# Performance work log

Hardware: AMD Instinct MI355X
Metric: run time of the kernel (lower is better)

## Reference

```python
import jax, jax.numpy as jnp
import numpy as np

N_NODES = 50000
N_EDGES = 600000
IN_FEATS = 128
OUT_FEATS = 128


def setup_inputs() -> dict:
    key = jax.random.key(0)
    k1, k2, k3, k4, k5 = jax.random.split(key, 5)
    edge_row = jax.random.randint(k1, (N_EDGES,), 0, N_NODES, dtype=jnp.int32)
    edge_col = jax.random.randint(k2, (N_EDGES,), 0, N_NODES, dtype=jnp.int32)
    edge_vals = jax.random.uniform(k3, (N_EDGES,), dtype=jnp.float32)
    node_embs = jax.random.normal(k4, (N_NODES, IN_FEATS), dtype=jnp.float32)
    gcn_weight = jax.random.normal(k5, (IN_FEATS, OUT_FEATS), dtype=jnp.float32) / np.sqrt(IN_FEATS)
    return {"edge_row": edge_row, "edge_col": edge_col, "edge_vals": edge_vals,
            "node_embs": node_embs, "gcn_weight": gcn_weight}


def reference(edge_row, edge_col, edge_vals, node_embs, gcn_weight):
    # SpMM: Ahat @ node_embs, with Ahat in COO form (row, col, val)
    gathered = node_embs[edge_col] * edge_vals[:, None]          # [E, in_feats]
    agg = jax.ops.segment_sum(gathered, edge_row, num_segments=N_NODES)  # [N, in_feats]
    # dense GEMM + activation
    out = jax.nn.relu(agg @ gcn_weight)                          # [N, out_feats]
    return out
```

## Files before the change

kernel.cpp:

```cpp
#include <hip/hip_runtime.h>
#include <hip/hip_fp16.h>

#define NN 50000
#define NE 600000
#define F  128
#define CAP 128
#define NFILL_BLK 586
#define NGEMM_BLK 782

#define WS_NEEDED 64200064u

__global__ void k_zero4(int4* __restrict__ p, int n4) {
    int i = blockIdx.x * blockDim.x + threadIdx.x;
    if (i < n4) p[i] = make_int4(0, 0, 0, 0);
}

#define FMA4(ACC, AS, WV) \
    ACC.x += (AS) * WV.x; ACC.y += (AS) * WV.y; ACC.z += (AS) * WV.z; ACC.w += (AS) * WV.w;

__global__ __launch_bounds__(256) void k_gemm_fill(const float* __restrict__ X,
                                                   const float* __restrict__ W,
                                                   __half* __restrict__ XW,
                                                   const int4* __restrict__ erow4,
                                                   const int4* __restrict__ ecol4,
                                                   const float4* __restrict__ eval4,
                                                   int* __restrict__ cnt,
                                                   int2* __restrict__ pairs) {
    if (blockIdx.x < NFILL_BLK) {
        int t = blockIdx.x * 256 + threadIdx.x;
        if (t * 4 < NE) {
            int4   r4 = erow4[t];
            int4   c4 = ecol4[t];
            float4 v4 = eval4[t];
            int p0 = atomicAdd(&cnt[r4.x], 1);
            int p1 = atomicAdd(&cnt[r4.y], 1);
            int p2 = atomicAdd(&cnt[r4.z], 1);
            int p3 = atomicAdd(&cnt[r4.w], 1);
            if (p0 < CAP) pairs[(size_t)r4.x * CAP + p0] = make_int2(c4.x, __float_as_int(v4.x));
            if (p1 < CAP) pairs[(size_t)r4.y * CAP + p1] = make_int2(c4.y, __float_as_int(v4.y));
            if (p2 < CAP) pairs[(size_t)r4.z * CAP + p2] = make_int2(c4.z, __float_as_int(v4.z));
            if (p3 < CAP) pairs[(size_t)r4.w * CAP + p3] = make_int2(c4.w, __float_as_int(v4.w));
        }
        return;
    }
    __shared__ float Wl[64][128];
    __shared__ float Al[64][128];
    const int tid = threadIdx.x;
    const int rg  = tid >> 5;
    const int oq  = (tid & 31) << 2;
    const int row0 = (blockIdx.x - NFILL_BLK) * 64;

    #pragma unroll
    for (int i = 0; i < 8; ++i) {
        int idx4 = i * 256 + tid;
        int r  = idx4 >> 5;
        int cc = (idx4 & 31) << 2;
        int grow = row0 + r;
        float4 v = make_float4(0.f, 0.f, 0.f, 0.f);
        if (grow < NN)
            v = *reinterpret_cast<const float4*>(X + (size_t)grow * F + cc);
        *reinterpret_cast<float4*>(&Al[r][cc]) = v;
    }

    float4 acc[8];
    #pragma unroll
    for (int j = 0; j < 8; ++j) acc[j] = make_float4(0.f, 0.f, 0.f, 0.f);

    for (int kk = 0; kk < 2; ++kk) {
        if (kk) __syncthreads();
        #pragma unroll
        for (int i = 0; i < 8; ++i) {
            int idx4 = i * 256 + tid;
            *reinterpret_cast<float4*>(reinterpret_cast<float*>(Wl) + idx4 * 4) =
                *reinterpret_cast<const float4*>(W + kk * 64 * F + idx4 * 4);
        }
        __syncthreads();
        #pragma unroll 2
        for (int k4 = 0; k4 < 64; k4 += 4) {
            float4 w0 = *reinterpret_cast<const float4*>(&Wl[k4 + 0][oq]);
            float4 w1 = *reinterpret_cast<const float4*>(&Wl[k4 + 1][oq]);
            float4 w2 = *reinterpret_cast<const float4*>(&Wl[k4 + 2][oq]);
            float4 w3 = *reinterpret_cast<const float4*>(&Wl[k4 + 3][oq]);
            #pragma unroll
            for (int r = 0; r < 8; ++r) {
                float4 a = *reinterpret_cast<const float4*>(&Al[rg * 8 + r][kk * 64 + k4]);
                FMA4(acc[r], a.x, w0)
                FMA4(acc[r], a.y, w1)
                FMA4(acc[r], a.z, w2)
                FMA4(acc[r], a.w, w3)
            }
        }
    }
    #pragma unroll
    for (int r = 0; r < 8; ++r) {
        int grow = row0 + rg * 8 + r;
        if (grow < NN) {
            float4 a = acc[r];
            __half2 lo = __float22half2_rn(make_float2(a.x, a.y));
            __half2 hi = __float22half2_rn(make_float2(a.z, a.w));
            uint2 pk;
            pk.x = *reinterpret_cast<unsigned*>(&lo);
            pk.y = *reinterpret_cast<unsigned*>(&hi);
            *reinterpret_cast<uint2*>(XW + (size_t)grow * F + oq) = pk;
        }
    }
}

#define PGATH(I, ACC) { \
    int2 e = bp[(I) + half]; \
    float v = __int_as_float(e.y); \
    uint2 h4 = *reinterpret_cast<const uint2*>(XW + (size_t)e.x * F + (li << 2)); \
    float2 flo = __half22float2(*reinterpret_cast<__half2*>(&h4.x)); \
    float2 fhi = __half22float2(*reinterpret_cast<__half2*>(&h4.y)); \
    ACC.x += flo.x * v; ACC.y += flo.y * v; ACC.z += fhi.x * v; ACC.w += fhi.y * v; }

__global__ __launch_bounds__(256) void k_agg_relu(const int* __restrict__ cnt,
                                                  const int2* __restrict__ pairs,
                                                  const __half* __restrict__ XW,
                                                  float* __restrict__ out) {
    const int wid  = threadIdx.x >> 6;
    const int lane = threadIdx.x & 63;
    const int node = blockIdx.x * 4 + wid;
    if (node >= NN) return;
    int n = cnt[node];
    n = (n > CAP) ? CAP : n;
    const int2* bp = pairs + (size_t)node * CAP;
    const int half = lane >> 5;
    const int li   = lane & 31;

    float4 a0 = make_float4(0.f, 0.f, 0.f, 0.f), a1 = a0, a2 = a0, a3 = a0;
    int i = 0;
    for (; i + 8 <= n; i += 8) {
        PGATH(i + 0, a0) PGATH(i + 2, a1) PGATH(i + 4, a2) PGATH(i + 6, a3)
    }
    if (i + 4 <= n) { PGATH(i + 0, a0) PGATH(i + 2, a1) i += 4; }
    if (i + 2 <= n) { PGATH(i + 0, a2) i += 2; }
    if (i < n) {
        int2 e = bp[i];
        float v = (half == 0) ? __int_as_float(e.y) : 0.f;
        uint2 h4 = *reinterpret_cast<const uint2*>(XW + (size_t)e.x * F + (li << 2));
        float2 flo = __half22float2(*reinterpret_cast<__half2*>(&h4.x));
        float2 fhi = __half22float2(*reinterpret_cast<__half2*>(&h4.y));
        a3.x += flo.x * v; a3.y += flo.y * v; a3.z += fhi.x * v; a3.w += fhi.y * v;
    }
    float4 s;
    s.x = (a0.x + a1.x) + (a2.x + a3.x);
    s.y = (a0.y + a1.y) + (a2.y + a3.y);
    s.z = (a0.z + a1.z) + (a2.z + a3.z);
    s.w = (a0.w + a1.w) + (a2.w + a3.w);
    s.x += __shfl_xor(s.x, 32);
    s.y += __shfl_xor(s.y, 32);
    s.z += __shfl_xor(s.z, 32);
    s.w += __shfl_xor(s.w, 32);
    if (half == 0) {
        s.x = fmaxf(s.x, 0.f);
        s.y = fmaxf(s.y, 0.f);
        s.z = fmaxf(s.z, 0.f);
        s.w = fmaxf(s.w, 0.f);
        *reinterpret_cast<float4*>(out + (size_t)node * F + (li << 2)) = s;
    }
}

__global__ void k_zero_f4(float4* __restrict__ p, int n4) {
    int i = blockIdx.x * blockDim.x + threadIdx.x;
    if (i < n4) p[i] = make_float4(0.f, 0.f, 0.f, 0.f);
}

__global__ void k_scatter(const int* __restrict__ erow, const int* __restrict__ ecol,
                          const float* __restrict__ eval, const float* __restrict__ X,
                          float* __restrict__ agg) {
    unsigned tid = blockIdx.x * blockDim.x + threadIdx.x;
    unsigned e = tid >> 5;
    if (e >= NE) return;
    unsigned f = (tid & 31u) << 2;
    int   r = erow[e];
    int   c = ecol[e];
    float v = eval[e];
    float4 x = *reinterpret_cast<const float4*>(X + (size_t)c * F + f);
    float* dst = agg + (size_t)r * F + f;
    atomicAdd(dst + 0, x.x * v);
    atomicAdd(dst + 1, x.y * v);
    atomicAdd(dst + 2, x.z * v);
    atomicAdd(dst + 3, x.w * v);
}

__global__ __launch_bounds__(256) void k_gemm_relu(float* __restrict__ io,
                                                   const float* __restrict__ W) {
    __shared__ float Wl[64][128];
    __shared__ float Al[64][128];
    const int tid = threadIdx.x;
    const int rg  = tid >> 5;
    const int oq  = (tid & 31) << 2;
    const int row0 = blockIdx.x * 64;

    #pragma unroll
    for (int i = 0; i < 8; ++i) {
        int idx4 = i * 256 + tid;
        int r  = idx4 >> 5;
        int cc = (idx4 & 31) << 2;
        int grow = row0 + r;
        float4 v = make_float4(0.f, 0.f, 0.f, 0.f);
        if (grow < NN)
            v = *reinterpret_cast<const float4*>(io + (size_t)grow * F + cc);
        *reinterpret_cast<float4*>(&Al[r][cc]) = v;
    }
    float4 acc[8];
    #pragma unroll
    for (int j = 0; j < 8; ++j) acc[j] = make_float4(0.f, 0.f, 0.f, 0.f);
    for (int kk = 0; kk < 2; ++kk) {
        if (kk) __syncthreads();
        #pragma unroll
        for (int i = 0; i < 8; ++i) {
            int idx4 = i * 256 + tid;
            *reinterpret_cast<float4*>(reinterpret_cast<float*>(Wl) + idx4 * 4) =
                *reinterpret_cast<const float4*>(W + kk * 64 * F + idx4 * 4);
        }
        __syncthreads();
        #pragma unroll 2
        for (int k4 = 0; k4 < 64; k4 += 4) {
            float4 w0 = *reinterpret_cast<const float4*>(&Wl[k4 + 0][oq]);
            float4 w1 = *reinterpret_cast<const float4*>(&Wl[k4 + 1][oq]);
            float4 w2 = *reinterpret_cast<const float4*>(&Wl[k4 + 2][oq]);
            float4 w3 = *reinterpret_cast<const float4*>(&Wl[k4 + 3][oq]);
            #pragma unroll
            for (int r = 0; r < 8; ++r) {
                float4 a = *reinterpret_cast<const float4*>(&Al[rg * 8 + r][kk * 64 + k4]);
                FMA4(acc[r], a.x, w0)
                FMA4(acc[r], a.y, w1)
                FMA4(acc[r], a.z, w2)
                FMA4(acc[r], a.w, w3)
            }
        }
    }
    #pragma unroll
    for (int r = 0; r < 8; ++r) {
        int grow = row0 + rg * 8 + r;
        if (grow < NN) {
            float4 a = acc[r];
            a.x = fmaxf(a.x, 0.f);
            a.y = fmaxf(a.y, 0.f);
            a.z = fmaxf(a.z, 0.f);
            a.w = fmaxf(a.w, 0.f);
            *reinterpret_cast<float4*>(io + (size_t)grow * F + oq) = a;
        }
    }
}

extern "C" void kernel_launch(void* const* d_in, const int* in_sizes, int n_in,
                              void* d_out, int out_size, void* d_ws, size_t ws_size,
                              hipStream_t stream) {
    const int*   erow  = (const int*)d_in[0];
    const int*   ecol  = (const int*)d_in[1];
    const float* evals = (const float*)d_in[2];
    const float* X     = (const float*)d_in[3];
    const float* W     = (const float*)d_in[4];
    float* out = (float*)d_out;

    if (ws_size >= WS_NEEDED) {
        char* ws = (char*)d_ws;
        int*    cnt   = (int*)(ws + 0);
        int2*   pairs = (int2*)(ws + 200064);
        __half* XW    = (__half*)(ws + 51400064);

        k_zero4<<<(NN / 4 + 255) / 256, 256, 0, stream>>>((int4*)cnt, NN / 4);
        k_gemm_fill<<<NFILL_BLK + NGEMM_BLK, 256, 0, stream>>>(
            X, W, XW, (const int4*)erow, (const int4*)ecol, (const float4*)evals,
            cnt, pairs);
        k_agg_relu<<<(NN + 3) / 4, 256, 0, stream>>>(cnt, pairs, XW, out);
    } else {
        const int n4 = NN * F / 4;
        k_zero_f4<<<(n4 + 255) / 256, 256, 0, stream>>>((float4*)out, n4);
        k_scatter<<<(NE * 32) / 256, 256, 0, stream>>>(erow, ecol, evals, X, out);
        k_gemm_relu<<<(NN + 63) / 64, 256, 0, stream>>>(out, W);
    }
}
```

Baseline: 95.52 us.

## Split fused gemm/fill kernel and fold count zeroing into GEMM kernel

Removes the separate zeroing kernel by zeroing the per-row counters inside the GEMM blocks. The edge-bucketing work moves out of the combined GEMM+fill launch into its own kernel that handles one edge per thread. This keeps the launch count at three but gives up the overlap of fill and GEMM inside one grid. The fill now depends on the GEMM launch finishing. Per-thread atomic work also becomes less vectorized.

```diff
diff --git a/kernel.cpp b/kernel.cpp
--- a/kernel.cpp
+++ b/kernel.cpp
@@ -5,50 +5,27 @@
 #define NE 600000
 #define F  128
 #define CAP 128
-#define NFILL_BLK 586
-#define NGEMM_BLK 782
 
 #define WS_NEEDED 64200064u
-
-__global__ void k_zero4(int4* __restrict__ p, int n4) {
-    int i = blockIdx.x * blockDim.x + threadIdx.x;
-    if (i < n4) p[i] = make_int4(0, 0, 0, 0);
-}
 
 #define FMA4(ACC, AS, WV) \
     ACC.x += (AS) * WV.x; ACC.y += (AS) * WV.y; ACC.z += (AS) * WV.z; ACC.w += (AS) * WV.w;
 
-__global__ __launch_bounds__(256) void k_gemm_fill(const float* __restrict__ X,
-                                                   const float* __restrict__ W,
-                                                   __half* __restrict__ XW,
-                                                   const int4* __restrict__ erow4,
-                                                   const int4* __restrict__ ecol4,
-                                                   const float4* __restrict__ eval4,
-                                                   int* __restrict__ cnt,
-                                                   int2* __restrict__ pairs) {
-    if (blockIdx.x < NFILL_BLK) {
-        int t = blockIdx.x * 256 + threadIdx.x;
-        if (t * 4 < NE) {
-            int4   r4 = erow4[t];
-            int4   c4 = ecol4[t];
-            float4 v4 = eval4[t];
-            int p0 = atomicAdd(&cnt[r4.x], 1);
-            int p1 = atomicAdd(&cnt[r4.y], 1);
-            int p2 = atomicAdd(&cnt[r4.z], 1);
-            int p3 = atomicAdd(&cnt[r4.w], 1);
-            if (p0 < CAP) pairs[(size_t)r4.x * CAP + p0] = make_int2(c4.x, __float_as_int(v4.x));
-            if (p1 < CAP) pairs[(size_t)r4.y * CAP + p1] = make_int2(c4.y, __float_as_int(v4.y));
-            if (p2 < CAP) pairs[(size_t)r4.z * CAP + p2] = make_int2(c4.z, __float_as_int(v4.z));
-            if (p3 < CAP) pairs[(size_t)r4.w * CAP + p3] = make_int2(c4.w, __float_as_int(v4.w));
-        }
-        return;
-    }
+__global__ __launch_bounds__(256) void k_gemm_xw(const float* __restrict__ X,
+                                                 const float* __restrict__ W,
+                                                 __half* __restrict__ XW,
+                                                 int* __restrict__ cnt) {
+    {
+        int gtid = blockIdx.x * 256 + threadIdx.x;
+        if (gtid < NN) cnt[gtid] = 0;
+    }
+
     __shared__ float Wl[64][128];
     __shared__ float Al[64][128];
     const int tid = threadIdx.x;
     const int rg  = tid >> 5;
     const int oq  = (tid & 31) << 2;
-    const int row0 = (blockIdx.x - NFILL_BLK) * 64;
+    const int row0 = blockIdx.x * 64;
 
     #pragma unroll
     for (int i = 0; i < 8; ++i) {
@@ -103,6 +80,18 @@
             pk.y = *reinterpret_cast<unsigned*>(&hi);
             *reinterpret_cast<uint2*>(XW + (size_t)grow * F + oq) = pk;
         }
+    }
+}
+
+__global__ void k_fill(const int* __restrict__ erow, const int* __restrict__ ecol,
+                       const float* __restrict__ eval, int* __restrict__ cnt,
+                       int2* __restrict__ pairs) {
+    int e = blockIdx.x * blockDim.x + threadIdx.x;
+    if (e < NE) {
+        int r = erow[e];
+        int p = atomicAdd(&cnt[r], 1);
+        if (p < CAP)
+            pairs[(size_t)r * CAP + p] = make_int2(ecol[e], __float_as_int(eval[e]));
     }
 }
 
@@ -262,10 +251,8 @@
         int2*   pairs = (int2*)(ws + 200064);
         __half* XW    = (__half*)(ws + 51400064);
 
-        k_zero4<<<(NN / 4 + 255) / 256, 256, 0, stream>>>((int4*)cnt, NN / 4);
-        k_gemm_fill<<<NFILL_BLK + NGEMM_BLK, 256, 0, stream>>>(
-            X, W, XW, (const int4*)erow, (const int4*)ecol, (const float4*)evals,
-            cnt, pairs);
+        k_gemm_xw<<<(NN + 63) / 64, 256, 0, stream>>>(X, W, XW, cnt);
+        k_fill<<<(NE + 255) / 256, 256, 0, stream>>>(erow, ecol, evals, cnt, pairs);
         k_agg_relu<<<(NN + 3) / 4, 256, 0, stream>>>(cnt, pairs, XW, out);
     } else {
         const int n4 = NN * F / 4;
```

Measured after the change: 97.55 us. +2.1%, slower.
